# Optimization experiments

Hardware: AMD Instinct MI355X
Metric: run time of the kernel (lower is better)

## Reference

```python
import jax, jax.numpy as jnp
import numpy as np

B, IN, H = 4096, 1024, 1024


def setup_inputs() -> dict:
    key = jax.random.key(0)
    ks = jax.random.split(key, 20)
    s_in = 1.0 / np.sqrt(IN)
    s_h = 1.0 / np.sqrt(H)
    def lin(kw, kb, fan_in, scale):
        W = jax.random.uniform(kw, (H, fan_in), jnp.float32, -scale, scale)
        b = jax.random.uniform(kb, (H,), jnp.float32, -scale, scale)
        return W, b
    Wxf, bxf = lin(ks[0], ks[1], IN, s_in)
    Whf, bhf = lin(ks[2], ks[3], H, s_h)
    Wxi, bxi = lin(ks[4], ks[5], IN, s_in)
    Whi, bhi = lin(ks[6], ks[7], H, s_h)
    Wxo, bxo = lin(ks[8], ks[9], IN, s_in)
    Who, bho = lin(ks[10], ks[11], H, s_h)
    Wxc, bxc = lin(ks[12], ks[13], IN, s_in)
    Whc, bhc = lin(ks[14], ks[15], H, s_h)
    x = jax.random.normal(ks[16], (B, IN), jnp.float32)
    c = jax.random.normal(ks[17], (B, H), jnp.float32)
    h = jax.random.normal(ks[18], (B, H), jnp.float32)
    return dict(x=x, c=c, h=h,
                Wxf=Wxf, bxf=bxf, Whf=Whf, bhf=bhf,
                Wxi=Wxi, bxi=bxi, Whi=Whi, bhi=bhi,
                Wxo=Wxo, bxo=bxo, Who=Who, bho=bho,
                Wxc=Wxc, bxc=bxc, Whc=Whc, bhc=bhc)


def reference(x, c, h,
              Wxf, bxf, Whf, bhf,
              Wxi, bxi, Whi, bhi,
              Wxo, bxo, Who, bho,
              Wxc, bxc, Whc, bhc):
    # Fuse the 8 small GEMMs into two batched GEMMs: x @ Wx^T and h @ Wh^T
    # with gate outputs concatenated along the hidden dim [f, i, o, c~].
    Wx = jnp.concatenate([Wxf, Wxi, Wxo, Wxc], axis=0)   # [4H, IN]
    Wh = jnp.concatenate([Whf, Whi, Who, Whc], axis=0)   # [4H, H]
    bx = jnp.concatenate([bxf, bxi, bxo, bxc], axis=0)   # [4H]
    bh = jnp.concatenate([bhf, bhi, bho, bhc], axis=0)   # [4H]
    gates = x @ Wx.T + h @ Wh.T + (bx + bh)              # [B, 4H]
    hs = Wxf.shape[0]
    f = jax.nn.sigmoid(gates[:, 0 * hs:1 * hs])
    i = jax.nn.sigmoid(gates[:, 1 * hs:2 * hs])
    o = jax.nn.sigmoid(gates[:, 2 * hs:3 * hs])
    ctil = jnp.tanh(gates[:, 3 * hs:4 * hs])
    ct = f * c + ctil * i
    ht = jnp.tanh(ct) * o
    return (ct, ht)
```

## Files before the change

### kernel.cpp

```cpp
#include <hip/hip_runtime.h>
#include <hip/hip_bf16.h>
#include <stdint.h>

typedef __hip_bfloat16 bf16;
typedef __attribute__((ext_vector_type(8))) short short8;
typedef __attribute__((ext_vector_type(4))) float floatx4;

#define AS1(p) ((const __attribute__((address_space(1))) void*)(p))
#define AS3(p) ((__attribute__((address_space(3))) void*)(p))

#define M_DIM 4096
#define H_DIM 1024

__device__ __forceinline__ unsigned short f2bf(float f) {
    uint32_t u = __float_as_uint(f);
    uint32_t r = (u + 0x7FFFu + ((u >> 16) & 1u)) >> 16;
    return (unsigned short)r;
}
__device__ __forceinline__ float fast_sigmoid(float v) {
    return 1.0f / (1.0f + __expf(-v));
}
__device__ __forceinline__ float fast_tanh(float v) {
    return 2.0f / (1.0f + __expf(-2.0f * v)) - 1.0f;
}

__global__ __launch_bounds__(256)
void pack_bf16(const float* __restrict__ x, const float* __restrict__ h,
               const float* Wxf, const float* Wxi, const float* Wxo, const float* Wxc,
               const float* Whf, const float* Whi, const float* Who, const float* Whc,
               unsigned short* __restrict__ ws)
{
    const int w = threadIdx.x >> 6;
    const int l = threadIdx.x & 63;
    const uint32_t W = blockIdx.x * 4u + (uint32_t)w;

    const uint32_t kg = (uint32_t)l >> 4;
    const uint32_t rr = (uint32_t)l & 15u;

    const float* src;
    uint32_t row, ktl;
    if (W < 16384u) {
        const uint32_t ch = W & 7u;
        const uint32_t KT = (W >> 3) & 63u;
        const uint32_t mx = W >> 9;
        src = (KT < 32u) ? x : h;
        ktl = KT & 31u;
        row = mx * 128u + ch * 16u + rr;
    } else {
        const uint32_t V  = W - 16384u;
        const uint32_t g  = V & 3u;
        const uint32_t KT = (V >> 2) & 63u;
        const uint32_t cc = (V >> 8) & 1u;
        const uint32_t ny = V >> 9;
        if (KT < 32u)
            src = (g == 0) ? Wxf : (g == 1) ? Wxi : (g == 2) ? Wxo : Wxc;
        else
            src = (g == 0) ? Whf : (g == 1) ? Whi : (g == 2) ? Who : Whc;
        ktl = KT & 31u;
        row = ny * 32u + cc * 16u + rr;
    }
    const float* s = src + (size_t)row * 1024u + ktl * 32u + kg * 8u;
    const float4 v0 = *(const float4*)s;
    const float4 v1 = *(const float4*)(s + 4);
    short8 pk;
    pk[0] = (short)f2bf(v0.x); pk[1] = (short)f2bf(v0.y);
    pk[2] = (short)f2bf(v0.z); pk[3] = (short)f2bf(v0.w);
    pk[4] = (short)f2bf(v1.x); pk[5] = (short)f2bf(v1.y);
    pk[6] = (short)f2bf(v1.z); pk[7] = (short)f2bf(v1.w);
    *(short8*)(ws + (size_t)W * 512u + (uint32_t)l * 8u) = pk;
}

#define GLL(srcp, dstp) __builtin_amdgcn_global_load_lds(AS1(srcp), AS3(dstp), 16, 0, 0)
#define WAITB(N) do {                                                          \
    asm volatile("s_waitcnt vmcnt(" #N ") lgkmcnt(0)\ns_barrier" ::: "memory");\
    __builtin_amdgcn_sched_barrier(0);                                         \
} while (0)

#define MFMA16(a, b, c) __builtin_amdgcn_mfma_f32_16x16x32_bf16((a), (b), (c), 0, 0, 0)

#define ISSUE_A(SL) do {                                                       \
    GLL(pA0, lds + (SL)*8192 + loffA);                                         \
    GLL(pA1, lds + (SL)*8192 + loffA + 1024);                                  \
    pA0 += 4096; pA1 += 4096;                                                  \
} while (0)

#define ISSUE_B(BB) do {                                                       \
    bb##BB##0 = *(const short8*)(pB);                                          \
    bb##BB##1 = *(const short8*)(pB + 512);                                    \
    bb##BB##2 = *(const short8*)(pB + 1024);                                   \
    bb##BB##3 = *(const short8*)(pB + 1536);                                   \
    pB += 2048;                                                                \
} while (0)

#define COMPUTE(SC, BB) do {                                                   \
    const short8 a0_ = *(const short8*)(ldsA + (SC)*8192 + 0);                 \
    const short8 a1_ = *(const short8*)(ldsA + (SC)*8192 + 1024);              \
    const short8 a2_ = *(const short8*)(ldsA + (SC)*8192 + 2048);              \
    const short8 a3_ = *(const short8*)(ldsA + (SC)*8192 + 3072);              \
    acc[0][0] = MFMA16(a0_, bb##BB##0, acc[0][0]);                             \
    acc[0][1] = MFMA16(a1_, bb##BB##0, acc[0][1]);                             \
    acc[0][2] = MFMA16(a2_, bb##BB##0, acc[0][2]);                             \
    acc[0][3] = MFMA16(a3_, bb##BB##0, acc[0][3]);                             \
    acc[1][0] = MFMA16(a0_, bb##BB##1, acc[1][0]);                             \
    acc[1][1] = MFMA16(a1_, bb##BB##1, acc[1][1]);                             \
    acc[1][2] = MFMA16(a2_, bb##BB##1, acc[1][2]);                             \
    acc[1][3] = MFMA16(a3_, bb##BB##1, acc[1][3]);                             \
    acc[2][0] = MFMA16(a0_, bb##BB##2, acc[2][0]);                             \
    acc[2][1] = MFMA16(a1_, bb##BB##2, acc[2][1]);                             \
    acc[2][2] = MFMA16(a2_, bb##BB##2, acc[2][2]);                             \
    acc[2][3] = MFMA16(a3_, bb##BB##2, acc[2][3]);                             \
    acc[3][0] = MFMA16(a0_, bb##BB##3, acc[3][0]);                             \
    acc[3][1] = MFMA16(a1_, bb##BB##3, acc[3][1]);                             \
    acc[3][2] = MFMA16(a2_, bb##BB##3, acc[3][2]);                             \
    acc[3][3] = MFMA16(a3_, bb##BB##3, acc[3][3]);                             \
} while (0)

#define ITER(SC, SL, CUR, NXT) do {                                            \
    WAITB(2);                                                                  \
    ISSUE_B(NXT);                                                              \
    ISSUE_A(SL);                                                               \
    COMPUTE(SC, CUR);                                                          \
} while (0)

__global__ __launch_bounds__(256, 2)
void lstm_fused_kernel(const unsigned short* __restrict__ ws,
                       const float* __restrict__ c,
                       const float* __restrict__ bxf, const float* __restrict__ bhf,
                       const float* __restrict__ bxi, const float* __restrict__ bhi,
                       const float* __restrict__ bxo, const float* __restrict__ bho,
                       const float* __restrict__ bxc, const float* __restrict__ bhc,
                       float* __restrict__ out)
{
    __shared__ __align__(16) char lds[3 * 8192];

    const int tid  = threadIdx.x;
    const int w    = tid >> 6;
    const int lane = tid & 63;

    const int bid  = blockIdx.x;
    const int wgid = (bid & 7) * 128 + (bid >> 3);
    const int ny  = wgid >> 5;
    const int mx  = wgid & 31;
    const int bm0 = mx * 128;
    const int bn0 = ny * 32;

    const int wM = w >> 1;
    const int wN = w & 1;

    const unsigned short* pA0 = ws + ((uint32_t)mx * 512u + (uint32_t)w * 2u) * 512u
                                   + (uint32_t)lane * 8u;
    const unsigned short* pA1 = pA0 + 512u;
    const uint32_t loffA = (uint32_t)w * 2048u;

    const unsigned short* pB = ws + 8388608u
                                  + ((uint32_t)(ny * 2 + wN)) * 131072u
                                  + (uint32_t)lane * 8u;

    const char* ldsA = lds + (uint32_t)wM * 4096u + (uint32_t)lane * 16u;

    short8 bb00, bb01, bb02, bb03;
    short8 bb10, bb11, bb12, bb13;

    floatx4 acc[4][4];
#pragma unroll
    for (int g = 0; g < 4; ++g)
#pragma unroll
        for (int mt = 0; mt < 4; ++mt)
            acc[g][mt] = (floatx4){0.f, 0.f, 0.f, 0.f};

    ISSUE_A(0);
    ISSUE_B(0);
    ISSUE_A(1);

    for (int t = 0; t < 10; ++t) {
        ITER(0, 2, 0, 1);
        ITER(1, 0, 1, 0);
        ITER(2, 1, 0, 1);
        ITER(0, 2, 1, 0);
        ITER(1, 0, 0, 1);
        ITER(2, 1, 1, 0);
    }
    ITER(0, 2, 0, 1);
    ITER(1, 0, 1, 0);
    WAITB(2); ISSUE_B(1); COMPUTE(2, 0);
    WAITB(0); COMPUTE(0, 1);

    const int lrc   = lane & 15;
    const int lquad = lane >> 4;
    const int colg  = bn0 + wN * 16 + lrc;
    const int wrow  = wM * 64;
    float* out_ct = out;
    float* out_ht = out + (size_t)M_DIM * H_DIM;

    const float bf_ = bxf[colg] + bhf[colg];
    const float bi_ = bxi[colg] + bhi[colg];
    const float bo_ = bxo[colg] + bho[colg];
    const float bc_ = bxc[colg] + bhc[colg];

#pragma unroll
    for (int mt = 0; mt < 4; ++mt) {
#pragma unroll
        for (int r = 0; r < 4; ++r) {
            const int row = bm0 + wrow + mt * 16 + lquad * 4 + r;
            const float f    = fast_sigmoid(acc[0][mt][r] + bf_);
            const float ii   = fast_sigmoid(acc[1][mt][r] + bi_);
            const float o    = fast_sigmoid(acc[2][mt][r] + bo_);
            const float ctil = fast_tanh(acc[3][mt][r] + bc_);
            const float cv   = c[(size_t)row * H_DIM + colg];
            const float ctn  = f * cv + ctil * ii;
            const float htn  = fast_tanh(ctn) * o;
            out_ct[(size_t)row * H_DIM + colg] = ctn;
            out_ht[(size_t)row * H_DIM + colg] = htn;
        }
    }
}

extern "C" void kernel_launch(void* const* d_in, const int* in_sizes, int n_in,
                              void* d_out, int out_size, void* d_ws, size_t ws_size,
                              hipStream_t stream) {
    (void)in_sizes; (void)n_in; (void)out_size; (void)ws_size;
    const float* x   = (const float*)d_in[0];
    const float* c   = (const float*)d_in[1];
    const float* h   = (const float*)d_in[2];
    const float* Wxf = (const float*)d_in[3];  const float* bxf = (const float*)d_in[4];
    const float* Whf = (const float*)d_in[5];  const float* bhf = (const float*)d_in[6];
    const float* Wxi = (const float*)d_in[7];  const float* bxi = (const float*)d_in[8];
    const float* Whi = (const float*)d_in[9];  const float* bhi = (const float*)d_in[10];
    const float* Wxo = (const float*)d_in[11]; const float* bxo = (const float*)d_in[12];
    const float* Who = (const float*)d_in[13]; const float* bho = (const float*)d_in[14];
    const float* Wxc = (const float*)d_in[15]; const float* bxc = (const float*)d_in[16];
    const float* Whc = (const float*)d_in[17]; const float* bhc = (const float*)d_in[18];
    float* out = (float*)d_out;
    unsigned short* ws = (unsigned short*)d_ws;

    pack_bf16<<<8192, 256, 0, stream>>>(x, h,
        Wxf, Wxi, Wxo, Wxc, Whf, Whi, Who, Whc, ws);

    lstm_fused_kernel<<<1024, 256, 0, stream>>>(ws, c,
        bxf, bhf, bxi, bhi, bxo, bho, bxc, bhc, out);
}
```

Before: 245.6 us.

## Widen block N tile to 64 columns and stage B operand through LDS

Each workgroup now covers 128 rows by 64 hidden columns across all four gates, halving the grid to 512 blocks. B (weight) tiles are now loaded into LDS with global_load_lds alongside A, replacing the per-wave direct global register loads. The pack kernel's weight layout is reordered to match the new 64-column tiling. This aims to cut A-tile reloads and global traffic per MFMA, at the cost of more LDS per stage (24 KB x3), more accumulators, and fewer workgroups, which may leave CUs underfilled.

Measured after the change: 506.6 us. 106% more time.

```diff
diff --git a/kernel.cpp b/kernel.cpp
--- a/kernel.cpp
+++ b/kernel.cpp
@@ -11,6 +11,7 @@
 
 #define M_DIM 4096
 #define H_DIM 1024
+#define STAGE 24576
 
 __device__ __forceinline__ unsigned short f2bf(float f) {
     uint32_t u = __float_as_uint(f);
@@ -48,16 +49,17 @@
         row = mx * 128u + ch * 16u + rr;
     } else {
         const uint32_t V  = W - 16384u;
-        const uint32_t g  = V & 3u;
-        const uint32_t KT = (V >> 2) & 63u;
-        const uint32_t cc = (V >> 8) & 1u;
-        const uint32_t ny = V >> 9;
+        const uint32_t b  = V & 15u;
+        const uint32_t KT = (V >> 4) & 63u;
+        const uint32_t ny = V >> 10;
+        const uint32_t g  = b >> 2;
+        const uint32_t c4 = b & 3u;
         if (KT < 32u)
             src = (g == 0) ? Wxf : (g == 1) ? Wxi : (g == 2) ? Wxo : Wxc;
         else
             src = (g == 0) ? Whf : (g == 1) ? Whi : (g == 2) ? Who : Whc;
         ktl = KT & 31u;
-        row = ny * 32u + cc * 16u + rr;
+        row = ny * 64u + c4 * 16u + rr;
     }
     const float* s = src + (size_t)row * 1024u + ktl * 32u + kg * 8u;
     const float4 v0 = *(const float4*)s;
@@ -78,49 +80,41 @@
 
 #define MFMA16(a, b, c) __builtin_amdgcn_mfma_f32_16x16x32_bf16((a), (b), (c), 0, 0, 0)
 
-#define ISSUE_A(SL) do {                                                       \
-    GLL(pA0, lds + (SL)*8192 + loffA);                                         \
-    GLL(pA1, lds + (SL)*8192 + loffA + 1024);                                  \
-    pA0 += 4096; pA1 += 4096;                                                  \
-} while (0)
-
-#define ISSUE_B(BB) do {                                                       \
-    bb##BB##0 = *(const short8*)(pB);                                          \
-    bb##BB##1 = *(const short8*)(pB + 512);                                    \
-    bb##BB##2 = *(const short8*)(pB + 1024);                                   \
-    bb##BB##3 = *(const short8*)(pB + 1536);                                   \
-    pB += 2048;                                                                \
-} while (0)
-
-#define COMPUTE(SC, BB) do {                                                   \
-    const short8 a0_ = *(const short8*)(ldsA + (SC)*8192 + 0);                 \
-    const short8 a1_ = *(const short8*)(ldsA + (SC)*8192 + 1024);              \
-    const short8 a2_ = *(const short8*)(ldsA + (SC)*8192 + 2048);              \
-    const short8 a3_ = *(const short8*)(ldsA + (SC)*8192 + 3072);              \
-    acc[0][0] = MFMA16(a0_, bb##BB##0, acc[0][0]);                             \
-    acc[0][1] = MFMA16(a1_, bb##BB##0, acc[0][1]);                             \
-    acc[0][2] = MFMA16(a2_, bb##BB##0, acc[0][2]);                             \
-    acc[0][3] = MFMA16(a3_, bb##BB##0, acc[0][3]);                             \
-    acc[1][0] = MFMA16(a0_, bb##BB##1, acc[1][0]);                             \
-    acc[1][1] = MFMA16(a1_, bb##BB##1, acc[1][1]);                             \
-    acc[1][2] = MFMA16(a2_, bb##BB##1, acc[1][2]);                             \
-    acc[1][3] = MFMA16(a3_, bb##BB##1, acc[1][3]);                             \
-    acc[2][0] = MFMA16(a0_, bb##BB##2, acc[2][0]);                             \
-    acc[2][1] = MFMA16(a1_, bb##BB##2, acc[2][1]);                             \
-    acc[2][2] = MFMA16(a2_, bb##BB##2, acc[2][2]);                             \
-    acc[2][3] = MFMA16(a3_, bb##BB##2, acc[2][3]);                             \
-    acc[3][0] = MFMA16(a0_, bb##BB##3, acc[3][0]);                             \
-    acc[3][1] = MFMA16(a1_, bb##BB##3, acc[3][1]);                             \
-    acc[3][2] = MFMA16(a2_, bb##BB##3, acc[3][2]);                             \
-    acc[3][3] = MFMA16(a3_, bb##BB##3, acc[3][3]);                             \
-} while (0)
-
-#define ITER(SC, SL, CUR, NXT) do {                                            \
-    WAITB(2);                                                                  \
-    ISSUE_B(NXT);                                                              \
-    ISSUE_A(SL);                                                               \
-    COMPUTE(SC, CUR);                                                          \
-} while (0)
+#define ISSUE(SL) do {                                                        \
+    GLL(p0, lds + (SL)*STAGE + lo0); p0 += ks0;                               \
+    GLL(p1, lds + (SL)*STAGE + lo1); p1 += ks1;                               \
+    GLL(p2, lds + (SL)*STAGE + lo2); p2 += ks2;                               \
+    GLL(p3, lds + (SL)*STAGE + lo3); p3 += ks3;                               \
+    GLL(p4, lds + (SL)*STAGE + lo4); p4 += ks4;                               \
+    GLL(p5, lds + (SL)*STAGE + lo5); p5 += ks5;                               \
+} while (0)
+
+#define QUAD(G, CC, BF)                                                       \
+    acc[G][CC][0] = MFMA16(a0_, BF, acc[G][CC][0]);                           \
+    acc[G][CC][1] = MFMA16(a1_, BF, acc[G][CC][1]);                           \
+    acc[G][CC][2] = MFMA16(a2_, BF, acc[G][CC][2]);                           \
+    acc[G][CC][3] = MFMA16(a3_, BF, acc[G][CC][3]);
+
+#define COMPUTE(SC) do {                                                      \
+    const short8 a0_ = *(const short8*)(ldsA + (SC)*STAGE + 0);               \
+    const short8 a1_ = *(const short8*)(ldsA + (SC)*STAGE + 1024);            \
+    const short8 a2_ = *(const short8*)(ldsA + (SC)*STAGE + 2048);            \
+    const short8 a3_ = *(const short8*)(ldsA + (SC)*STAGE + 3072);            \
+    const short8 b00_ = *(const short8*)(ldsB + (SC)*STAGE + 0);              \
+    const short8 b01_ = *(const short8*)(ldsB + (SC)*STAGE + 1024);           \
+    const short8 b10_ = *(const short8*)(ldsB + (SC)*STAGE + 4096);           \
+    const short8 b11_ = *(const short8*)(ldsB + (SC)*STAGE + 4096 + 1024);    \
+    const short8 b20_ = *(const short8*)(ldsB + (SC)*STAGE + 8192);           \
+    const short8 b21_ = *(const short8*)(ldsB + (SC)*STAGE + 8192 + 1024);    \
+    const short8 b30_ = *(const short8*)(ldsB + (SC)*STAGE + 12288);          \
+    const short8 b31_ = *(const short8*)(ldsB + (SC)*STAGE + 12288 + 1024);   \
+    QUAD(0, 0, b00_) QUAD(0, 1, b01_)                                         \
+    QUAD(1, 0, b10_) QUAD(1, 1, b11_)                                         \
+    QUAD(2, 0, b20_) QUAD(2, 1, b21_)                                         \
+    QUAD(3, 0, b30_) QUAD(3, 1, b31_)                                         \
+} while (0)
+
+#define ITER(SC, SL) do { WAITB(6); ISSUE(SL); COMPUTE(SC); } while (0)
 
 __global__ __launch_bounds__(256, 2)
 void lstm_fused_kernel(const unsigned short* __restrict__ ws,
@@ -131,86 +125,96 @@
                        const float* __restrict__ bxc, const float* __restrict__ bhc,
                        float* __restrict__ out)
 {
-    __shared__ __align__(16) char lds[3 * 8192];
+    __shared__ __align__(16) char lds[3 * STAGE];
 
     const int tid  = threadIdx.x;
     const int w    = tid >> 6;
     const int lane = tid & 63;
 
-    const int bid  = blockIdx.x;
-    const int wgid = (bid & 7) * 128 + (bid >> 3);
-    const int ny  = wgid >> 5;
-    const int mx  = wgid & 31;
+    const int bid = blockIdx.x;
+    const int mx  = bid >> 4;
+    const int ny  = ((bid & 7) << 1) | ((bid >> 3) & 1);
     const int bm0 = mx * 128;
-    const int bn0 = ny * 32;
+    const int bn0 = ny * 64;
 
     const int wM = w >> 1;
-    const int wN = w & 1;
-
-    const unsigned short* pA0 = ws + ((uint32_t)mx * 512u + (uint32_t)w * 2u) * 512u
-                                   + (uint32_t)lane * 8u;
-    const unsigned short* pA1 = pA0 + 512u;
-    const uint32_t loffA = (uint32_t)w * 2048u;
-
-    const unsigned short* pB = ws + 8388608u
-                                  + ((uint32_t)(ny * 2 + wN)) * 131072u
-                                  + (uint32_t)lane * 8u;
-
-    const char* ldsA = lds + (uint32_t)wM * 4096u + (uint32_t)lane * 16u;
-
-    short8 bb00, bb01, bb02, bb03;
-    short8 bb10, bb11, bb12, bb13;
-
-    floatx4 acc[4][4];
+    const int wc = w & 1;
+
+    const unsigned short* p0; const unsigned short* p1; const unsigned short* p2;
+    const unsigned short* p3; const unsigned short* p4; const unsigned short* p5;
+    uint32_t lo0, lo1, lo2, lo3, lo4, lo5, ks0, ks1, ks2, ks3, ks4, ks5;
+#define CHDEC(CH, P, LO, KS) do {                                             \
+    const uint32_t ch_ = (uint32_t)(CH);                                      \
+    if (ch_ < 8u) {                                                           \
+        P  = ws + ((uint32_t)mx * 512u + ch_) * 512u + (uint32_t)lane * 8u;   \
+        KS = 8u * 512u;                                                       \
+    } else {                                                                  \
+        const uint32_t b_ = ch_ - 8u;                                         \
+        P  = ws + (16384u + (uint32_t)ny * 1024u + b_) * 512u                 \
+                + (uint32_t)lane * 8u;                                        \
+        KS = 16u * 512u;                                                      \
+    }                                                                         \
+    LO = ch_ * 1024u;                                                         \
+} while (0)
+    CHDEC(w * 6 + 0, p0, lo0, ks0);
+    CHDEC(w * 6 + 1, p1, lo1, ks1);
+    CHDEC(w * 6 + 2, p2, lo2, ks2);
+    CHDEC(w * 6 + 3, p3, lo3, ks3);
+    CHDEC(w * 6 + 4, p4, lo4, ks4);
+    CHDEC(w * 6 + 5, p5, lo5, ks5);
+#undef CHDEC
+
+    const char* ldsA = lds + (uint32_t)lane * 16u + (uint32_t)wM * 4096u;
+    const char* ldsB = lds + (uint32_t)lane * 16u + 8192u + (uint32_t)wc * 2048u;
+
+    floatx4 acc[4][2][4];
 #pragma unroll
     for (int g = 0; g < 4; ++g)
 #pragma unroll
-        for (int mt = 0; mt < 4; ++mt)
-            acc[g][mt] = (floatx4){0.f, 0.f, 0.f, 0.f};
-
-    ISSUE_A(0);
-    ISSUE_B(0);
-    ISSUE_A(1);
-
-    for (int t = 0; t < 10; ++t) {
-        ITER(0, 2, 0, 1);
-        ITER(1, 0, 1, 0);
-        ITER(2, 1, 0, 1);
-        ITER(0, 2, 1, 0);
-        ITER(1, 0, 0, 1);
-        ITER(2, 1, 1, 0);
+        for (int cc = 0; cc < 2; ++cc)
+#pragma unroll
+            for (int mt = 0; mt < 4; ++mt)
+                acc[g][cc][mt] = (floatx4){0.f, 0.f, 0.f, 0.f};
+
+    ISSUE(0);
+    ISSUE(1);
+
+    for (int t = 0; t < 20; ++t) {
+        ITER(0, 2); ITER(1, 0); ITER(2, 1);
     }
-    ITER(0, 2, 0, 1);
-    ITER(1, 0, 1, 0);
-    WAITB(2); ISSUE_B(1); COMPUTE(2, 0);
-    WAITB(0); COMPUTE(0, 1);
+    ITER(0, 2);
+    ITER(1, 0);
+    WAITB(6); COMPUTE(2);
+    WAITB(0); COMPUTE(0);
 
     const int lrc   = lane & 15;
     const int lquad = lane >> 4;
-    const int colg  = bn0 + wN * 16 + lrc;
     const int wrow  = wM * 64;
     float* out_ct = out;
     float* out_ht = out + (size_t)M_DIM * H_DIM;
 
-    const float bf_ = bxf[colg] + bhf[colg];
-    const float bi_ = bxi[colg] + bhi[colg];
-    const float bo_ = bxo[colg] + bho[colg];
-    const float bc_ = bxc[colg] + bhc[colg];
-
-#pragma unroll
-    for (int mt = 0; mt < 4; ++mt) {
-#pragma unroll
-        for (int r = 0; r < 4; ++r) {
-            const int row = bm0 + wrow + mt * 16 + lquad * 4 + r;
-            const float f    = fast_sigmoid(acc[0][mt][r] + bf_);
-            const float ii   = fast_sigmoid(acc[1][mt][r] + bi_);
-            const float o    = fast_sigmoid(acc[2][mt][r] + bo_);
-            const float ctil = fast_tanh(acc[3][mt][r] + bc_);
-            const float cv   = c[(size_t)row * H_DIM + colg];
-            const float ctn  = f * cv + ctil * ii;
-            const float htn  = fast_tanh(ctn) * o;
-            out_ct[(size_t)row * H_DIM + colg] = ctn;
-            out_ht[(size_t)row * H_DIM + colg] = htn;
+#pragma unroll
+    for (int cc = 0; cc < 2; ++cc) {
+        const int colg = bn0 + wc * 32 + cc * 16 + lrc;
+        const float bf_ = bxf[colg] + bhf[colg];
+        const float bi_ = bxi[colg] + bhi[colg];
+        const float bo_ = bxo[colg] + bho[colg];
+        const float bc_ = bxc[colg] + bhc[colg];
+#pragma unroll
+        for (int mt = 0; mt < 4; ++mt) {
+#pragma unroll
+            for (int r = 0; r < 4; ++r) {
+                const int row = bm0 + wrow + mt * 16 + lquad * 4 + r;
+                const float f    = fast_sigmoid(acc[0][cc][mt][r] + bf_);
+                const float ii   = fast_sigmoid(acc[1][cc][mt][r] + bi_);
+                const float o    = fast_sigmoid(acc[2][cc][mt][r] + bo_);
+                const float ctil = fast_tanh(acc[3][cc][mt][r] + bc_);
+                const float cv   = c[(size_t)row * H_DIM + colg];
+                const float ctn  = f * cv + ctil * ii;
+                const float htn  = fast_tanh(ctn) * o;
+                out_ct[(size_t)row * H_DIM + colg] = ctn;
+                out_ht[(size_t)row * H_DIM + colg] = htn;
+            }
         }
     }
 }
@@ -236,6 +240,6 @@
     pack_bf16<<<8192, 256, 0, stream>>>(x, h,
         Wxf, Wxi, Wxo, Wxc, Whf, Whi, Who, Whc, ws);
 
-    lstm_fused_kernel<<<1024, 256, 0, stream>>>(ws, c,
+    lstm_fused_kernel<<<512, 256, 0, stream>>>(ws, c,
         bxf, bhf, bxi, bhi, bxo, bho, bxc, bhc, out);
 }
```
